# Optimization experiments

Measured on AMD Instinct MI355X. Metric: run time of the kernel, lower is better.

## Reference

```python
import jax, jax.numpy as jnp
import numpy as np

NEG_INF = -1e20  # neginf(float32) as in ParlAI


def setup_inputs() -> dict:
    key = jax.random.key(0)
    k1, k2, k3 = jax.random.split(key, 3)
    B, XL, YL, D = 16, 1024, 1024, 1024
    xs = jax.random.normal(k1, (B, XL, D), dtype=jnp.float32)
    ys = jax.random.normal(k2, (B, YL, D), dtype=jnp.float32)
    mask_ys = jax.random.randint(k3, (B, YL), 0, 2, dtype=jnp.int32)
    return {"xs": xs, "ys": ys, "mask_ys": mask_ys}


def reference(xs, ys, mask_ys):
    # scores: [B, x_len, y_len] = xs @ ys^T (no scaling, matching the module)
    scores = jnp.einsum('bxd,byd->bxy', xs, ys)
    # mask positions where mask_ys == 0, broadcast over query dim
    scores = jnp.where((mask_ys == 0)[:, None, :], NEG_INF, scores)
    weight = jax.nn.softmax(scores, axis=2)
    emb = jnp.einsum('bxy,byd->bxd', weight, ys)
    return (emb, weight)
```

## Files before the change

kernel.cpp:

```cpp
#include <hip/hip_runtime.h>
#include <hip/hip_bf16.h>
#include <stdint.h>

#define NBATCH 16
#define NDIM   1024
#define NEL    (16u*1024u*1024u)

typedef __attribute__((ext_vector_type(8))) short bf16x8;
typedef __attribute__((ext_vector_type(4))) short short4_t;
typedef __attribute__((ext_vector_type(4))) float f32x4;
typedef __attribute__((ext_vector_type(4))) int   i32x4;

__device__ __forceinline__ short f2bf(float f){
  union { __hip_bfloat16 b; short s; } u;
  u.b = __float2bfloat16(f);
  return u.s;
}
__device__ __forceinline__ float bf2f(short s){
  union { short s; __hip_bfloat16 b; } u;
  u.s = s;
  return __bfloat162float(u.b);
}

__global__ __launch_bounds__(256) void k_split(const float* __restrict__ in,
                                               short* __restrict__ hi,
                                               short* __restrict__ lo)
{
  const size_t i = ((size_t)blockIdx.x * 256 + threadIdx.x) * 4;
  f32x4 v = *(const f32x4*)(in + i);
  short4_t h, l;
  #pragma unroll
  for (int j = 0; j < 4; j++){
    short hb = f2bf(v[j]);
    h[j] = hb;
    l[j] = f2bf(v[j] - bf2f(hb));
  }
  *(short4_t*)(hi + i) = h;
  *(short4_t*)(lo + i) = l;
}

__global__ __launch_bounds__(256) void k_transpose(const float* __restrict__ ys,
                                                   short* __restrict__ ysT)
{
  __shared__ float t[32][33];
  const int b = blockIdx.z;
  const int y0 = blockIdx.y * 32;
  const int d0 = blockIdx.x * 32;
  const float* src = ys + ((size_t)b * NDIM + y0) * NDIM + d0;
  #pragma unroll
  for (int r = threadIdx.y; r < 32; r += 8)
    t[r][threadIdx.x] = src[(size_t)r * NDIM + threadIdx.x];
  __syncthreads();
  short* dst = ysT + ((size_t)b * NDIM + d0) * NDIM + y0;
  #pragma unroll
  for (int r = threadIdx.y; r < 32; r += 8)
    dst[(size_t)r * NDIM + threadIdx.x] = f2bf(t[threadIdx.x][r]);
}

__device__ __forceinline__ void gload_lds16(const short* g, short* l){
  __builtin_amdgcn_global_load_lds((const __attribute__((address_space(1))) void*)g,
                                   (__attribute__((address_space(3))) void*)l,
                                   16, 0, 0);
}

template<int SPLIT>
__global__ __launch_bounds__(256, 2) void k_gemm_bt(
    const short* __restrict__ Ahi, const short* __restrict__ Alo,
    const short* __restrict__ Bhi, const short* __restrict__ Blo,
    float* __restrict__ C)
{
  constexpr int NT = SPLIT ? 4 : 2;
  constexpr int TB = SPLIT ? 2 : 1;
  __shared__ __align__(16) short lds[2][NT][128 * 32];

  const int tid  = threadIdx.x;
  const int lane = tid & 63;
  const int wid  = tid >> 6;
  const int wr   = wid >> 1;
  const int wc   = wid & 1;

  const size_t bofs = (size_t)blockIdx.z * NDIM * NDIM;
  const short* A0 = Ahi + bofs + (size_t)blockIdx.x * 128 * NDIM;
  const short* B0 = Bhi + bofs + (size_t)blockIdx.y * 128 * NDIM;
  const short* A1 = nullptr; const short* B1 = nullptr;
  if constexpr (SPLIT){
    A1 = Alo + bofs + (size_t)blockIdx.x * 128 * NDIM;
    B1 = Blo + bofs + (size_t)blockIdx.y * 128 * NDIM;
  }

  auto stage = [&](int buf, int kt){
    #pragma unroll
    for (int i = 0; i < 2; i++){
      const int grow = i * 64 + (tid >> 2);
      const int slot = (tid & 3) ^ ((grow >> 1) & 3);
      const size_t go = (size_t)grow * NDIM + kt * 32 + slot * 8;
      const int lofs = i * 2048 + wid * 512;
      gload_lds16(A0 + go, &lds[buf][0][0] + lofs);
      gload_lds16(B0 + go, &lds[buf][TB][0] + lofs);
      if constexpr (SPLIT){
        gload_lds16(A1 + go, &lds[buf][1][0] + lofs);
        gload_lds16(B1 + go, &lds[buf][3][0] + lofs);
      }
    }
  };

  auto rfrag = [&](const short* t, int row) -> bf16x8 {
    const int p = (lane >> 4) ^ ((row >> 1) & 3);
    return *(const bf16x8*)(t + row * 32 + p * 8);
  };

  f32x4 acc[4][4] = {};

  stage(0, 0);
  __syncthreads();

  for (int kt = 0; kt < 32; ++kt){
    const int cur = kt & 1;
    if (kt < 31) stage(cur ^ 1, kt + 1);

    bf16x8 ah[4], bh[4], al[4], bl[4];
    #pragma unroll
    for (int m = 0; m < 4; m++){
      const int r = wr * 64 + m * 16 + (lane & 15);
      ah[m] = rfrag(&lds[cur][0][0], r);
      if constexpr (SPLIT) al[m] = rfrag(&lds[cur][1][0], r);
    }
    #pragma unroll
    for (int n = 0; n < 4; n++){
      const int r = wc * 64 + n * 16 + (lane & 15);
      bh[n] = rfrag(&lds[cur][TB][0], r);
      if constexpr (SPLIT) bl[n] = rfrag(&lds[cur][3][0], r);
    }
    #pragma unroll
    for (int m = 0; m < 4; m++){
      #pragma unroll
      for (int n = 0; n < 4; n++){
        acc[m][n] = __builtin_amdgcn_mfma_f32_16x16x32_bf16(ah[m], bh[n], acc[m][n], 0, 0, 0);
        if constexpr (SPLIT){
          acc[m][n] = __builtin_amdgcn_mfma_f32_16x16x32_bf16(ah[m], bl[n], acc[m][n], 0, 0, 0);
          acc[m][n] = __builtin_amdgcn_mfma_f32_16x16x32_bf16(al[m], bh[n], acc[m][n], 0, 0, 0);
        }
      }
    }
    __syncthreads();
  }

  float* Cb = C + bofs;
  const int row0 = blockIdx.x * 128 + wr * 64 + (lane >> 4) * 4;
  const int col0 = blockIdx.y * 128 + wc * 64 + (lane & 15);
  #pragma unroll
  for (int m = 0; m < 4; m++)
    #pragma unroll
    for (int n = 0; n < 4; n++)
      #pragma unroll
      for (int r = 0; r < 4; r++)
        Cb[(size_t)(row0 + m * 16 + r) * NDIM + col0 + n * 16] = acc[m][n][r];
}

__global__ __launch_bounds__(256) void k_softmax(float* __restrict__ w,
                                                 short* __restrict__ wbf,
                                                 const int* __restrict__ mask)
{
  const int gw   = blockIdx.x * 4 + (threadIdx.x >> 6);
  const int b    = gw >> 10;
  const int x    = gw & 1023;
  const int lane = threadIdx.x & 63;
  float* row  = w   + ((size_t)b * NDIM + x) * NDIM;
  short* rowb = wbf + ((size_t)b * NDIM + x) * NDIM;
  const int* mrow = mask + b * NDIM;

  f32x4 v[4]; i32x4 mk[4];
  float mx = -INFINITY;
  #pragma unroll
  for (int j = 0; j < 4; j++){
    const int c = j * 256 + lane * 4;
    v[j]  = *(const f32x4*)(row + c);
    mk[j] = *(const i32x4*)(mrow + c);
    #pragma unroll
    for (int e = 0; e < 4; e++)
      if (mk[j][e]) mx = fmaxf(mx, v[j][e]);
  }
  #pragma unroll
  for (int off = 32; off >= 1; off >>= 1) mx = fmaxf(mx, __shfl_xor(mx, off));

  float sum = 0.f;
  #pragma unroll
  for (int j = 0; j < 4; j++)
    #pragma unroll
    for (int e = 0; e < 4; e++){
      const float p = mk[j][e] ? __expf(v[j][e] - mx) : 0.f;
      v[j][e] = p; sum += p;
    }
  #pragma unroll
  for (int off = 32; off >= 1; off >>= 1) sum += __shfl_xor(sum, off);
  const float inv = sum > 0.f ? 1.f / sum : 0.f;

  #pragma unroll
  for (int j = 0; j < 4; j++){
    const int c = j * 256 + lane * 4;
    f32x4 o; short4_t ob;
    #pragma unroll
    for (int e = 0; e < 4; e++){
      const float p = v[j][e] * inv;
      o[e] = p; ob[e] = f2bf(p);
    }
    *(f32x4*)(row + c)  = o;
    *(short4_t*)(rowb + c) = ob;
  }
}

extern "C" void kernel_launch(void* const* d_in, const int* in_sizes, int n_in,
                              void* d_out, int out_size, void* d_ws, size_t ws_size,
                              hipStream_t stream)
{
  const float* xs   = (const float*)d_in[0];
  const float* ys   = (const float*)d_in[1];
  const int*   mask = (const int*)d_in[2];

  float* emb = (float*)d_out;
  float* wgt = emb + (size_t)NEL;

  short* xs_hi = (short*)d_ws;
  short* xs_lo = xs_hi + NEL;
  short* ys_hi = xs_lo + NEL;
  short* ys_lo = ys_hi + NEL;
  short* ysT   = ys_lo + NEL;
  short* w_bf  = xs_hi;

  k_split<<<NEL / 1024, 256, 0, stream>>>(xs, xs_hi, xs_lo);
  k_split<<<NEL / 1024, 256, 0, stream>>>(ys, ys_hi, ys_lo);
  k_transpose<<<dim3(32, 32, NBATCH), dim3(32, 8), 0, stream>>>(ys, ysT);
  k_gemm_bt<1><<<dim3(8, 8, NBATCH), 256, 0, stream>>>(xs_hi, xs_lo, ys_hi, ys_lo, wgt);
  k_softmax<<<(NBATCH * NDIM) / 4, 256, 0, stream>>>(wgt, w_bf, mask);
  k_gemm_bt<0><<<dim3(8, 8, NBATCH), 256, 0, stream>>>(w_bf, nullptr, ysT, nullptr, emb);
}
```

Measured before the change: 450.4 us.

## Use 256x256-tile GEMM with 4-stage pipeline and fuse ys split with transpose

Replaces the 128x128 GEMM with a 512-thread 256x256 tile kernel. The split-bf16 products are handled as three concatenated K segments (hi*hi, hi*lo, lo*hi) over a four-deep LDS ring, with explicit waitcnt, barriers and priority control, plus a swizzled block ordering. The ys hi/lo split and the transpose are fused into one kernel, so ys is read once. The goal is more operand reuse per LDS load, better load/compute overlap and fewer memory passes, at the cost of only 256 blocks and fragile hand-written synchronisation.

```diff
diff --git a/kernel.cpp b/kernel.cpp
--- a/kernel.cpp
+++ b/kernel.cpp
@@ -39,22 +39,33 @@
   *(short4_t*)(lo + i) = l;
 }
 
-__global__ __launch_bounds__(256) void k_transpose(const float* __restrict__ ys,
+__global__ __launch_bounds__(512) void k_split_ysT(const float* __restrict__ ys,
+                                                   short* __restrict__ hi,
+                                                   short* __restrict__ lo,
                                                    short* __restrict__ ysT)
 {
-  __shared__ float t[32][33];
-  const int b = blockIdx.z;
-  const int y0 = blockIdx.y * 32;
-  const int d0 = blockIdx.x * 32;
+  __shared__ float t[64][65];
+  const int b  = blockIdx.z;
+  const int y0 = blockIdx.y * 64;
+  const int d0 = blockIdx.x * 64;
+  const int lx = threadIdx.x;
+  const int ly = threadIdx.y;
   const float* src = ys + ((size_t)b * NDIM + y0) * NDIM + d0;
-  #pragma unroll
-  for (int r = threadIdx.y; r < 32; r += 8)
-    t[r][threadIdx.x] = src[(size_t)r * NDIM + threadIdx.x];
+  short* ph = hi + ((size_t)b * NDIM + y0) * NDIM + d0;
+  short* pl = lo + ((size_t)b * NDIM + y0) * NDIM + d0;
+  #pragma unroll
+  for (int r = ly; r < 64; r += 8){
+    float v = src[(size_t)r * NDIM + lx];
+    short hb = f2bf(v);
+    ph[(size_t)r * NDIM + lx] = hb;
+    pl[(size_t)r * NDIM + lx] = f2bf(v - bf2f(hb));
+    t[r][lx] = v;
+  }
   __syncthreads();
-  short* dst = ysT + ((size_t)b * NDIM + d0) * NDIM + y0;
-  #pragma unroll
-  for (int r = threadIdx.y; r < 32; r += 8)
-    dst[(size_t)r * NDIM + threadIdx.x] = f2bf(t[threadIdx.x][r]);
+  short* pt = ysT + ((size_t)b * NDIM + d0) * NDIM + y0;
+  #pragma unroll
+  for (int r = ly; r < 64; r += 8)
+    pt[(size_t)r * NDIM + lx] = f2bf(t[lx][r]);
 }
 
 __device__ __forceinline__ void gload_lds16(const short* g, short* l){
@@ -63,93 +74,114 @@
                                    16, 0, 0);
 }
 
-template<int SPLIT>
-__global__ __launch_bounds__(256, 2) void k_gemm_bt(
-    const short* __restrict__ Ahi, const short* __restrict__ Alo,
-    const short* __restrict__ Bhi, const short* __restrict__ Blo,
-    float* __restrict__ C)
-{
-  constexpr int NT = SPLIT ? 4 : 2;
-  constexpr int TB = SPLIT ? 2 : 1;
-  __shared__ __align__(16) short lds[2][NT][128 * 32];
+#define MFMA_BF16(d, a, b) d = __builtin_amdgcn_mfma_f32_16x16x32_bf16(a, b, d, 0, 0, 0)
+
+__global__ __launch_bounds__(512, 2) void k_gemm256(
+    const short* __restrict__ A0, const short* __restrict__ A1, const short* __restrict__ A2,
+    const short* __restrict__ B0, const short* __restrict__ B1, const short* __restrict__ B2,
+    float* __restrict__ C, int nt)
+{
+  __shared__ __align__(16) short lds[4][2][2][4096];
 
   const int tid  = threadIdx.x;
   const int lane = tid & 63;
   const int wid  = tid >> 6;
-  const int wr   = wid >> 1;
-  const int wc   = wid & 1;
-
-  const size_t bofs = (size_t)blockIdx.z * NDIM * NDIM;
-  const short* A0 = Ahi + bofs + (size_t)blockIdx.x * 128 * NDIM;
-  const short* B0 = Bhi + bofs + (size_t)blockIdx.y * 128 * NDIM;
-  const short* A1 = nullptr; const short* B1 = nullptr;
-  if constexpr (SPLIT){
-    A1 = Alo + bofs + (size_t)blockIdx.x * 128 * NDIM;
-    B1 = Blo + bofs + (size_t)blockIdx.y * 128 * NDIM;
-  }
-
-  auto stage = [&](int buf, int kt){
-    #pragma unroll
-    for (int i = 0; i < 2; i++){
-      const int grow = i * 64 + (tid >> 2);
-      const int slot = (tid & 3) ^ ((grow >> 1) & 3);
-      const size_t go = (size_t)grow * NDIM + kt * 32 + slot * 8;
-      const int lofs = i * 2048 + wid * 512;
-      gload_lds16(A0 + go, &lds[buf][0][0] + lofs);
-      gload_lds16(B0 + go, &lds[buf][TB][0] + lofs);
-      if constexpr (SPLIT){
-        gload_lds16(A1 + go, &lds[buf][1][0] + lofs);
-        gload_lds16(B1 + go, &lds[buf][3][0] + lofs);
-      }
+  const int wr   = wid >> 2;
+  const int wcl  = wid & 3;
+
+  const int lid = blockIdx.x;
+  const int swz = (lid & 7) * 32 + (lid >> 3);
+  const int bz = swz >> 4, by = (swz >> 2) & 3, bx = swz & 3;
+
+  const size_t bofs = (size_t)bz * NDIM * NDIM;
+  const size_t arow = (size_t)bx * 256 * NDIM;
+  const size_t brow = (size_t)by * 256 * NDIM;
+  const short* Ap0 = A0 + bofs + arow; const short* Ap1 = A1 + bofs + arow;
+  const short* Ap2 = A2 + bofs + arow;
+  const short* Bp0 = B0 + bofs + brow; const short* Bp1 = B1 + bofs + brow;
+  const short* Bp2 = B2 + bofs + brow;
+
+  const int srow = tid >> 2;
+  const int sslot = (tid & 3) ^ ((srow >> 1) & 3);
+
+  auto stageT = [&](int kt, int sel){
+    const int r = kt & 3;
+    const int seg = kt >> 5;
+    const int k0 = (kt & 31) * 32;
+    const short* P = sel ? (seg == 0 ? Bp0 : (seg == 1 ? Bp1 : Bp2))
+                         : (seg == 0 ? Ap0 : (seg == 1 ? Ap1 : Ap2));
+    short* dbase = &lds[r][sel][0][0] + wid * 512;
+    #pragma unroll
+    for (int h = 0; h < 2; h++)
+      gload_lds16(P + (size_t)(h * 128 + srow) * NDIM + k0 + sslot * 8,
+                  dbase + h * 4096);
+  };
+
+  auto rdA = [&](int kt, int m) -> bf16x8 {
+    const int rl = m * 16 + (lane & 15);
+    const int p  = (lane >> 4) ^ ((rl >> 1) & 3);
+    return *(const bf16x8*)(&lds[kt & 3][0][wr][0] + rl * 32 + p * 8);
+  };
+  auto rdB = [&](int kt, int n) -> bf16x8 {
+    const int rb = wcl * 64 + n * 16 + (lane & 15);
+    const int p  = (lane >> 4) ^ ((rb >> 1) & 3);
+    return *(const bf16x8*)(&lds[kt & 3][1][rb >> 7][0] + (rb & 127) * 32 + p * 8);
+  };
+
+  f32x4 acc[8][4] = {};
+
+  stageT(0, 0); stageT(0, 1);
+  stageT(1, 0); stageT(1, 1);
+  stageT(2, 0); stageT(2, 1);
+  asm volatile("s_waitcnt vmcnt(8)" ::: "memory");
+  __builtin_amdgcn_s_barrier();
+
+  for (int t = 0; t < nt; ++t){
+    bf16x8 af[4], bfr[4];
+    #pragma unroll
+    for (int m = 0; m < 4; m++) af[m] = rdA(t, m);
+    #pragma unroll
+    for (int n = 0; n < 4; n++) bfr[n] = rdB(t, n);
+    if (t + 3 < nt) stageT(t + 3, 0);
+    __builtin_amdgcn_s_barrier();
+    asm volatile("s_waitcnt lgkmcnt(0)" ::: "memory");
+    __builtin_amdgcn_sched_barrier(0);
+    __builtin_amdgcn_s_setprio(1);
+    #pragma unroll
+    for (int m = 0; m < 4; m++)
+      #pragma unroll
+      for (int n = 0; n < 4; n++)
+        MFMA_BF16(acc[m][n], af[m], bfr[n]);
+    __builtin_amdgcn_s_setprio(0);
+    __builtin_amdgcn_s_barrier();
+
+    bf16x8 ag[4];
+    #pragma unroll
+    for (int m = 0; m < 4; m++) ag[m] = rdA(t, m + 4);
+    if (t + 3 < nt) stageT(t + 3, 1);
+    if (t + 1 < nt){
+      if (t + 3 < nt)      asm volatile("s_waitcnt vmcnt(8)" ::: "memory");
+      else if (t + 2 < nt) asm volatile("s_waitcnt vmcnt(4)" ::: "memory");
+      else                 asm volatile("s_waitcnt vmcnt(0)" ::: "memory");
     }
-  };
-
-  auto rfrag = [&](const short* t, int row) -> bf16x8 {
-    const int p = (lane >> 4) ^ ((row >> 1) & 3);
-    return *(const bf16x8*)(t + row * 32 + p * 8);
-  };
-
-  f32x4 acc[4][4] = {};
-
-  stage(0, 0);
-  __syncthreads();
-
-  for (int kt = 0; kt < 32; ++kt){
-    const int cur = kt & 1;
-    if (kt < 31) stage(cur ^ 1, kt + 1);
-
-    bf16x8 ah[4], bh[4], al[4], bl[4];
-    #pragma unroll
-    for (int m = 0; m < 4; m++){
-      const int r = wr * 64 + m * 16 + (lane & 15);
-      ah[m] = rfrag(&lds[cur][0][0], r);
-      if constexpr (SPLIT) al[m] = rfrag(&lds[cur][1][0], r);
-    }
-    #pragma unroll
-    for (int n = 0; n < 4; n++){
-      const int r = wc * 64 + n * 16 + (lane & 15);
-      bh[n] = rfrag(&lds[cur][TB][0], r);
-      if constexpr (SPLIT) bl[n] = rfrag(&lds[cur][3][0], r);
-    }
-    #pragma unroll
-    for (int m = 0; m < 4; m++){
+    __builtin_amdgcn_s_barrier();
+    asm volatile("s_waitcnt lgkmcnt(0)" ::: "memory");
+    __builtin_amdgcn_sched_barrier(0);
+    __builtin_amdgcn_s_setprio(1);
+    #pragma unroll
+    for (int m = 0; m < 4; m++)
       #pragma unroll
-      for (int n = 0; n < 4; n++){
-        acc[m][n] = __builtin_amdgcn_mfma_f32_16x16x32_bf16(ah[m], bh[n], acc[m][n], 0, 0, 0);
-        if constexpr (SPLIT){
-          acc[m][n] = __builtin_amdgcn_mfma_f32_16x16x32_bf16(ah[m], bl[n], acc[m][n], 0, 0, 0);
-          acc[m][n] = __builtin_amdgcn_mfma_f32_16x16x32_bf16(al[m], bh[n], acc[m][n], 0, 0, 0);
-        }
-      }
-    }
-    __syncthreads();
+      for (int n = 0; n < 4; n++)
+        MFMA_BF16(acc[m + 4][n], ag[m], bfr[n]);
+    __builtin_amdgcn_s_setprio(0);
+    __builtin_amdgcn_s_barrier();
   }
 
   float* Cb = C + bofs;
-  const int row0 = blockIdx.x * 128 + wr * 64 + (lane >> 4) * 4;
-  const int col0 = blockIdx.y * 128 + wc * 64 + (lane & 15);
-  #pragma unroll
-  for (int m = 0; m < 4; m++)
+  const int row0 = bx * 256 + wr * 128 + (lane >> 4) * 4;
+  const int col0 = by * 256 + wcl * 64 + (lane & 15);
+  #pragma unroll
+  for (int m = 0; m < 8; m++)
     #pragma unroll
     for (int n = 0; n < 4; n++)
       #pragma unroll
@@ -228,9 +260,10 @@
   short* w_bf  = xs_hi;
 
   k_split<<<NEL / 1024, 256, 0, stream>>>(xs, xs_hi, xs_lo);
-  k_split<<<NEL / 1024, 256, 0, stream>>>(ys, ys_hi, ys_lo);
-  k_transpose<<<dim3(32, 32, NBATCH), dim3(32, 8), 0, stream>>>(ys, ysT);
-  k_gemm_bt<1><<<dim3(8, 8, NBATCH), 256, 0, stream>>>(xs_hi, xs_lo, ys_hi, ys_lo, wgt);
+  k_split_ysT<<<dim3(16, 16, NBATCH), dim3(64, 8), 0, stream>>>(ys, ys_hi, ys_lo, ysT);
+  k_gemm256<<<256, 512, 0, stream>>>(xs_hi, xs_hi, xs_lo,
+                                     ys_hi, ys_lo, ys_hi, wgt, 96);
   k_softmax<<<(NBATCH * NDIM) / 4, 256, 0, stream>>>(wgt, w_bf, mask);
-  k_gemm_bt<0><<<dim3(8, 8, NBATCH), 256, 0, stream>>>(w_bf, nullptr, ysT, nullptr, emb);
-}
+  k_gemm256<<<256, 512, 0, stream>>>(w_bf, w_bf, w_bf,
+                                     ysT, ysT, ysT, emb, 32);
+}
```

Measured after the change: 404.9 us. 10.1% less time.
